# Kernel optimization log

Measured on AMD Instinct MI355X. Metric: run time of the kernel, lower is better.

The kernel has to match this reference:

```python
import jax, jax.numpy as jnp
import numpy as np
import math

K_HISTORY = 32  # sliding-window length over GRU hidden states


def rotate_half(x):
    half = x.shape[-1] // 2
    return jnp.concatenate([-x[..., half:], x[..., :half]], axis=-1)


def setup_inputs() -> dict:
    key = jax.random.key(0)
    ks = jax.random.split(key, 8)
    B, MB, IN = 8, 512, 1024          # batch, max_bin, input_size (gru_hidden_size)
    EMB, H, KVH, HD, BS = 1024, 16, 4, 64, 16  # embed_dim, heads, kv_heads, head_dim, bin_size
    h = jax.random.normal(ks[0], (B, MB, IN), jnp.float32)
    # RoPE tables: rotate-half layout, theta repeated over both halves
    pos = jnp.arange(MB, dtype=jnp.float32)
    inv_freq = 1.0 / (10000.0 ** (jnp.arange(0, HD, 2, dtype=jnp.float32) / HD))
    theta = pos[:, None] * inv_freq[None, :]            # (MB, HD/2)
    theta = jnp.concatenate([theta, theta], axis=-1)    # (MB, HD)
    freqs_cos = jnp.cos(theta)
    freqs_sin = jnp.sin(theta)
    s = 0.02
    Wq = jax.random.normal(ks[1], (EMB, H * HD), jnp.float32) * s
    Wk = jax.random.normal(ks[2], (IN, KVH * HD), jnp.float32) * s
    Wv = jax.random.normal(ks[3], (IN, KVH * HD), jnp.float32) * s
    Wo = jax.random.normal(ks[4], (H * HD, EMB), jnp.float32) * s
    output_queries = jax.random.normal(ks[5], (BS, EMB), jnp.float32)
    Wr = jax.random.normal(ks[6], (EMB, 2), jnp.float32) * s
    br = jnp.zeros((2,), jnp.float32)
    return {"h": h, "freqs_cos": freqs_cos, "freqs_sin": freqs_sin,
            "Wq": Wq, "Wk": Wk, "Wv": Wv, "Wo": Wo,
            "output_queries": output_queries, "Wr": Wr, "br": br}


def reference(h, freqs_cos, freqs_sin, Wq, Wk, Wv, Wo, output_queries, Wr, br):
    B, MB, IN = h.shape
    HD = freqs_cos.shape[1]
    H = Wq.shape[1] // HD
    KVH = Wk.shape[1] // HD
    n_rep = H // KVH
    BS = output_queries.shape[0]
    K = K_HISTORY

    # sliding windows over bins: window t covers h[t-K+1 : t+1] (zero left-pad)
    h_padded = jnp.concatenate([jnp.zeros((B, K - 1, IN), h.dtype), h], axis=1)
    idx = jnp.arange(MB)[:, None] + jnp.arange(K)[None, :]   # (MB, K)
    h_win = h_padded[:, idx, :]                              # (B, MB, K, IN)

    k = (h_win @ Wk).reshape(B, MB, K, KVH, HD)
    v = (h_win @ Wv).reshape(B, MB, K, KVH, HD)

    # queries: shared learned output queries, identical across batch & bins
    q = (output_queries @ Wq).reshape(BS, H, HD)             # (BS, H, HD)
    # RoPE on Q only (is_decoder=True) at within-bin offsets 0..BS-1
    offs = jnp.arange(BS)
    cos = freqs_cos[offs][:, None, :]                        # (BS, 1, HD)
    sin = freqs_sin[offs][:, None, :]
    q = q * cos + rotate_half(q) * sin                       # (BS, H, HD)

    # GQA: repeat_interleave KV heads to H heads
    k = jnp.repeat(k, n_rep, axis=3)                         # (B, MB, K, H, HD)
    v = jnp.repeat(v, n_rep, axis=3)

    scores = jnp.einsum("qhd,bmkhd->bmhqk", q, k) / math.sqrt(HD)
    attn = jax.nn.softmax(scores, axis=-1)                   # (B, MB, H, BS, K)
    attn_out = jnp.einsum("bmhqk,bmkhd->bmqhd", attn, v)
    attn_out = attn_out.reshape(B, MB, BS, H * HD)

    z = attn_out @ Wo                                        # (B, MB, BS, EMB)
    vel = z @ Wr + br                                        # (B, MB, BS, 2)
    return vel.reshape(B, MB * BS, 2)
```

## Files before the change

kernel.cpp:

```cpp
#include <hip/hip_runtime.h>


typedef __attribute__((ext_vector_type(8))) short v8s;
typedef __attribute__((ext_vector_type(4))) short v4sh;
typedef __attribute__((ext_vector_type(4))) float v4f;

#define OFF_WOR  0u
#define OFF_QR   2048u
#define OFF_WTH  18432u
#define OFF_WTL  182272u
#define OFF_S0   346112u
#define OFF_S1   1460224u
#define OFF_VW0  2574336u
#define OFF_VW1  2713600u
#define SROW 544

__device__ __forceinline__ void split_bf16(float a, unsigned short& h, unsigned short& l) {
    const unsigned u = __float_as_uint(a);
    h = (unsigned short)(u >> 16);
    const float r = a - __uint_as_float(u & 0xFFFF0000u);
    unsigned v = __float_as_uint(r);
    v += 0x7FFFu + ((v >> 16) & 1u);
    l = (unsigned short)(v >> 16);
}

__global__ __launch_bounds__(256) void kP(
    const float* __restrict__ oq, const float* __restrict__ Wq,
    const float* __restrict__ fc, const float* __restrict__ fs,
    const float* __restrict__ Wo, const float* __restrict__ Wr,
    float* __restrict__ qr, float* __restrict__ Wor,
    float* __restrict__ S0, float* __restrict__ S1,
    float* __restrict__ VW0, float* __restrict__ VW1,
    unsigned* __restrict__ wthu, unsigned* __restrict__ wtlu)
{
    __shared__ float sm[2048];
    const int b = blockIdx.x, t = threadIdx.x;
    if (b < 256) {
        const int q = b >> 4, h = b & 15;
        #pragma unroll
        for (int j = 0; j < 4; ++j) sm[t + 256 * j] = oq[q * 1024 + t + 256 * j];
        __syncthreads();
        const int w = t >> 6, lane = t & 63;
        const float* wq = Wq + (size_t)(w * 256) * 1024 + h * 64 + lane;
        const float* os = sm + w * 256;
        float acc = 0.f;
        #pragma unroll 16
        for (int e = 0; e < 256; ++e) acc = fmaf(os[e], wq[(size_t)e * 1024], acc);
        sm[1024 + w * 64 + lane] = acc;
        __syncthreads();
        if (t < 64) {
            const int d = t, p = d ^ 32;
            const float a1 = sm[1024 + d] + sm[1088 + d] + sm[1152 + d] + sm[1216 + d];
            const float a2 = sm[1024 + p] + sm[1088 + p] + sm[1152 + p] + sm[1216 + p];
            const float c = fc[q * 64 + d], s = fs[q * 64 + d];
            const float rh = (d < 32) ? -a2 : a2;
            qr[q * 1024 + h * 64 + d] = fmaf(a1, c, rh * s);
        }
    } else if (b < 512) {
        #pragma unroll
        for (int j = 0; j < 8; ++j) sm[t + 256 * j] = Wr[t + 256 * j];
        __syncthreads();
        const int i = (b - 256) * 4 + (t >> 6);
        const int lane = t & 63;
        float a0 = 0.f, a1 = 0.f;
        const float* wo = Wo + (size_t)i * 1024 + lane;
        #pragma unroll
        for (int j = 0; j < 16; ++j) {
            const float w = wo[j * 64];
            const int e = lane + j * 64;
            a0 = fmaf(w, sm[2 * e], a0);
            a1 = fmaf(w, sm[2 * e + 1], a1);
        }
        #pragma unroll
        for (int w = 1; w < 64; w <<= 1) {
            a0 += __shfl_xor(a0, w, 64);
            a1 += __shfl_xor(a1, w, 64);
        }
        if (lane == 0) { Wor[i * 2] = a0; Wor[i * 2 + 1] = a1; }
    } else if (b < 656) {
        const int idx = (b - 512) * 256 + t;
        const float4 z = make_float4(0.f, 0.f, 0.f, 0.f);
        if (idx < 16384)       *(float4*)(S0  + (size_t)(idx >> 3) * SROW + (idx & 7) * 4) = z;
        else if (idx < 32768)  *(float4*)(S1  + (size_t)((idx - 16384) >> 3) * SROW + (idx & 7) * 4) = z;
        else if (idx < 34816)  *(float4*)(VW0 + (size_t)((idx - 32768) >> 3) * SROW + (idx & 7) * 4) = z;
        else                   *(float4*)(VW1 + (size_t)((idx - 34816) >> 3) * SROW + (idx & 7) * 4) = z;
    } else {
        unsigned* dst = (b == 656) ? wthu : wtlu;
        #pragma unroll
        for (int j = 0; j < 64; ++j) dst[147456 + t + 256 * j] = 0u;
    }
}

__global__ __launch_bounds__(256) void kW(
    const float* __restrict__ Wk, const float* __restrict__ Wv,
    const float* __restrict__ qr, const float* __restrict__ Wor,
    unsigned short* __restrict__ Wth, unsigned short* __restrict__ Wtl)
{
    __shared__ float As[32 * 68];
    __shared__ float Bt[72 * 68];
    const int b = blockIdx.x, t = threadIdx.x;
    const int g = b >> 5, i0 = (b & 31) * 32;
    #pragma unroll
    for (int jj = 0; jj < 16; ++jj) {
        const int i2 = t + 256 * jj;
        const int d = i2 & 63, col = i2 >> 6;
        Bt[col * 68 + d] = qr[(col >> 2) * 1024 + (g * 4 + (col & 3)) * 64 + d];
    }
    #pragma unroll
    for (int jj = 0; jj < 2; ++jj) {
        const int i2 = t + 256 * jj;
        const int d = i2 & 63, vc = i2 >> 6;
        Bt[(64 + vc) * 68 + d] = Wor[((g * 4 + (vc >> 1)) * 64 + d) * 2 + (vc & 1)];
    }
    {
        const int i = t >> 3, dc = (t & 7) * 8;
        const float* src = Wk + (size_t)(i0 + i) * 256 + g * 64 + dc;
        *(float4*)&As[i * 68 + dc] = *(const float4*)src;
        *(float4*)&As[i * 68 + dc + 4] = *(const float4*)(src + 4);
    }
    __syncthreads();
    const int jc = t & 63, iq = t >> 6;
    {
        float out[8];
        #pragma unroll
        for (int r = 0; r < 8; ++r) out[r] = 0.f;
        #pragma unroll
        for (int dc = 0; dc < 16; ++dc) {
            const float4 bv = *(const float4*)&Bt[jc * 68 + dc * 4];
            #pragma unroll
            for (int r = 0; r < 8; ++r) {
                const float4 av = *(const float4*)&As[(iq * 8 + r) * 68 + dc * 4];
                out[r] = fmaf(av.x, bv.x, out[r]);
                out[r] = fmaf(av.y, bv.y, out[r]);
                out[r] = fmaf(av.z, bv.z, out[r]);
                out[r] = fmaf(av.w, bv.w, out[r]);
            }
        }
        const int j = (jc >> 2) * 16 + g * 4 + (jc & 3);
        v8s ph, pl;
        #pragma unroll
        for (int r = 0; r < 8; ++r) {
            unsigned short hh, ll;
            split_bf16(out[r] * 0.125f, hh, ll);
            ph[r] = (short)hh; pl[r] = (short)ll;
        }
        *(v8s*)&Wth[(size_t)j * 1024 + i0 + iq * 8] = ph;
        *(v8s*)&Wtl[(size_t)j * 1024 + i0 + iq * 8] = pl;
    }
    __syncthreads();
    {
        const int i = t >> 3, dc = (t & 7) * 8;
        const float* src = Wv + (size_t)(i0 + i) * 256 + g * 64 + dc;
        *(float4*)&As[i * 68 + dc] = *(const float4*)src;
        *(float4*)&As[i * 68 + dc + 4] = *(const float4*)(src + 4);
    }
    __syncthreads();
    {
        const int il = t >> 3, vc = t & 7;
        float acc = 0.f;
        #pragma unroll
        for (int dc = 0; dc < 16; ++dc) {
            const float4 av = *(const float4*)&As[il * 68 + dc * 4];
            const float4 bv = *(const float4*)&Bt[(64 + vc) * 68 + dc * 4];
            acc = fmaf(av.x, bv.x, acc);
            acc = fmaf(av.y, bv.y, acc);
            acc = fmaf(av.z, bv.z, acc);
            acc = fmaf(av.w, bv.w, acc);
        }
        const int j = 256 + (g * 4 + (vc >> 1)) * 2 + (vc & 1);
        unsigned short hh, ll;
        split_bf16(acc, hh, ll);
        Wth[(size_t)j * 1024 + i0 + il] = hh;
        Wtl[(size_t)j * 1024 + i0 + il] = ll;
    }
}

__global__ __launch_bounds__(256) void k2(
    const float* __restrict__ A,
    const unsigned short* __restrict__ Wth, const unsigned short* __restrict__ Wtl,
    float* __restrict__ S0, float* __restrict__ S1,
    float* __restrict__ VW0, float* __restrict__ VW1)
{
    __shared__ unsigned short Ah[64 * 72], Al[64 * 72];
    __shared__ unsigned short Bh[64 * 72], Bl[64 * 72];
    const int m0 = blockIdx.x * 64;
    const int n0 = blockIdx.y * 64;
    const int kh = blockIdx.z;
    const int t = threadIdx.x;
    const int lane = t & 63, wv = t >> 6;
    const int l16 = lane & 15, quad = lane >> 4;
    const int wm = wv >> 1, wn = wv & 1;
    const int sr = t >> 2, kc = (t & 3) * 8;
    v4f acc[2][2];
    #pragma unroll
    for (int i = 0; i < 2; ++i)
        #pragma unroll
        for (int j = 0; j < 2; ++j) acc[i][j] = (v4f)(0.f);
    const float* Ap = A + (size_t)(m0 + sr) * 1024 + kh * 512 + kc;
    const unsigned short* Bph = Wth + (size_t)(n0 + sr) * 1024 + kh * 512 + kc;
    const unsigned short* Bpl = Wtl + (size_t)(n0 + sr) * 1024 + kh * 512 + kc;
    for (int k0 = 0; k0 < 512; k0 += 64) {
        const float4 a00 = *(const float4*)(Ap + k0);
        const float4 a01 = *(const float4*)(Ap + k0 + 4);
        const float4 a10 = *(const float4*)(Ap + k0 + 32);
        const float4 a11 = *(const float4*)(Ap + k0 + 36);
        const v8s bh0 = *(const v8s*)(Bph + k0);
        const v8s bh1 = *(const v8s*)(Bph + k0 + 32);
        const v8s bl0 = *(const v8s*)(Bpl + k0);
        const v8s bl1 = *(const v8s*)(Bpl + k0 + 32);
        v8s ah0, al0, ah1, al1;
        {
            const float af0[8] = {a00.x, a00.y, a00.z, a00.w, a01.x, a01.y, a01.z, a01.w};
            const float af1[8] = {a10.x, a10.y, a10.z, a10.w, a11.x, a11.y, a11.z, a11.w};
            #pragma unroll
            for (int j = 0; j < 8; ++j) {
                unsigned short hh, ll;
                split_bf16(af0[j], hh, ll);
                ah0[j] = (short)hh; al0[j] = (short)ll;
                split_bf16(af1[j], hh, ll);
                ah1[j] = (short)hh; al1[j] = (short)ll;
            }
        }
        __syncthreads();
        *(v8s*)&Ah[sr * 72 + kc] = ah0;  *(v8s*)&Ah[sr * 72 + kc + 32] = ah1;
        *(v8s*)&Al[sr * 72 + kc] = al0;  *(v8s*)&Al[sr * 72 + kc + 32] = al1;
        *(v8s*)&Bh[sr * 72 + kc] = bh0;  *(v8s*)&Bh[sr * 72 + kc + 32] = bh1;
        *(v8s*)&Bl[sr * 72 + kc] = bl0;  *(v8s*)&Bl[sr * 72 + kc + 32] = bl1;
        __syncthreads();
        #pragma unroll
        for (int kk = 0; kk < 2; ++kk) {
            v8s fah[2], fal[2], fbh[2], fbl[2];
            #pragma unroll
            for (int s = 0; s < 2; ++s) {
                const int mr = wm * 32 + s * 16 + l16;
                fah[s] = *(const v8s*)&Ah[mr * 72 + kk * 32 + quad * 8];
                fal[s] = *(const v8s*)&Al[mr * 72 + kk * 32 + quad * 8];
                const int nr = wn * 32 + s * 16 + l16;
                fbh[s] = *(const v8s*)&Bh[nr * 72 + kk * 32 + quad * 8];
                fbl[s] = *(const v8s*)&Bl[nr * 72 + kk * 32 + quad * 8];
            }
            #pragma unroll
            for (int ms = 0; ms < 2; ++ms)
                #pragma unroll
                for (int ns = 0; ns < 2; ++ns) {
                    acc[ms][ns] = __builtin_amdgcn_mfma_f32_16x16x32_bf16(fal[ms], fbh[ns], acc[ms][ns], 0, 0, 0);
                    acc[ms][ns] = __builtin_amdgcn_mfma_f32_16x16x32_bf16(fah[ms], fbl[ns], acc[ms][ns], 0, 0, 0);
                    acc[ms][ns] = __builtin_amdgcn_mfma_f32_16x16x32_bf16(fah[ms], fbh[ns], acc[ms][ns], 0, 0, 0);
                }
        }
    }
    float* Sh  = kh ? S1 : S0;
    float* VWh = kh ? VW1 : VW0;
    #pragma unroll
    for (int ms = 0; ms < 2; ++ms)
        #pragma unroll
        for (int ns = 0; ns < 2; ++ns) {
            const int j = n0 + wn * 32 + ns * 16 + l16;
            if (j >= 288) continue;
            const int m = m0 + wm * 32 + ms * 16 + quad * 4;
            const int bb = m >> 9, tt = m & 511;
            const float4 v = make_float4(acc[ms][ns][0], acc[ms][ns][1], acc[ms][ns][2], acc[ms][ns][3]);
            float* dst;
            if (j < 256)
                dst = Sh + (size_t)((bb * 16 + (j >> 4)) * 16 + (j & 15)) * SROW + 32 + tt;
            else
                dst = VWh + (size_t)(bb * 32 + (j - 256)) * SROW + 32 + tt;
            *(float4*)dst = v;
        }
}

__global__ __launch_bounds__(256) void k3(
    const float* __restrict__ S0, const float* __restrict__ S1,
    const float* __restrict__ VW0, const float* __restrict__ VW1,
    const float* __restrict__ brp, float* __restrict__ out)
{
    __shared__ float Es[16 * 164];
    __shared__ float EVs[32 * 164];
    const int b = blockIdx.x, q = blockIdx.y, qt = blockIdx.z;
    const int tbase = qt * 128;
    const int t = threadIdx.x;
    for (int idx = t; idx < 640; idx += 256) {
        const int h = idx / 40, g = idx - h * 40;
        const size_t off = (size_t)((b * 16 + q) * 16 + h) * SROW + tbase + g * 4;
        const float4 a = *(const float4*)(S0 + off);
        const float4 c = *(const float4*)(S1 + off);
        float4 e;
        e.x = __expf(a.x + c.x); e.y = __expf(a.y + c.y);
        e.z = __expf(a.z + c.z); e.w = __expf(a.w + c.w);
        *(float4*)(Es + h * 164 + g * 4) = e;
    }
    __syncthreads();
    for (int idx = t; idx < 1280; idx += 256) {
        const int hc = idx / 40, g = idx - hc * 40;
        const size_t off = (size_t)(b * 32 + hc) * SROW + tbase + g * 4;
        const float4 v0 = *(const float4*)(VW0 + off);
        const float4 v1 = *(const float4*)(VW1 + off);
        const float4 e = *(const float4*)(Es + (hc >> 1) * 164 + g * 4);
        float4 rr;
        rr.x = e.x * (v0.x + v1.x); rr.y = e.y * (v0.y + v1.y);
        rr.z = e.z * (v0.z + v1.z); rr.w = e.w * (v0.w + v1.w);
        *(float4*)(EVs + hc * 164 + g * 4) = rr;
    }
    __syncthreads();
    const int h = t & 15, mg = t >> 4;
    const float* ep = Es + h * 164 + mg * 8;
    const float* e0 = EVs + (2 * h) * 164 + mg * 8;
    const float* e1 = EVs + (2 * h + 1) * 164 + mg * 8;
    float den = 0.f, n0s = 0.f, n1s = 0.f;
    #pragma unroll
    for (int s = 0; s < 32; ++s) {
        const int ss = 1 + ((s + 2 * h) & 31);
        den += ep[ss]; n0s += e0[ss]; n1s += e1[ss];
    }
    const float br0 = brp[0], br1 = brp[1];
    #pragma unroll
    for (int u = 0; u < 8; ++u) {
        const float inv = __builtin_amdgcn_rcpf(den);
        float c0 = n0s * inv, c1 = n1s * inv;
        #pragma unroll
        for (int w = 1; w < 16; w <<= 1) {
            c0 += __shfl_xor(c0, w, 64);
            c1 += __shfl_xor(c1, w, 64);
        }
        if (h == 0) {
            const int m = tbase + mg * 8 + u;
            float* o = out + (size_t)((b * 512 + m) * 16 + q) * 2;
            o[0] = c0 + br0;
            o[1] = c1 + br1;
        }
        if (u < 7) {
            den += ep[33 + u] - ep[1 + u];
            n0s += e0[33 + u] - e0[1 + u];
            n1s += e1[33 + u] - e1[1 + u];
        }
    }
}

extern "C" void kernel_launch(void* const* d_in, const int* in_sizes, int n_in,
                              void* d_out, int out_size, void* d_ws, size_t ws_size,
                              hipStream_t stream)
{
    (void)in_sizes; (void)n_in; (void)out_size; (void)ws_size;
    const float* h  = (const float*)d_in[0];
    const float* fc = (const float*)d_in[1];
    const float* fs = (const float*)d_in[2];
    const float* Wq = (const float*)d_in[3];
    const float* Wk = (const float*)d_in[4];
    const float* Wv = (const float*)d_in[5];
    const float* Wo = (const float*)d_in[6];
    const float* oq = (const float*)d_in[7];
    const float* Wr = (const float*)d_in[8];
    const float* br = (const float*)d_in[9];
    float* ws = (float*)d_ws;
    float* Wor  = ws + OFF_WOR;
    float* qr   = ws + OFF_QR;
    unsigned short* Wth = (unsigned short*)(ws + OFF_WTH);
    unsigned short* Wtl = (unsigned short*)(ws + OFF_WTL);
    float* S0   = ws + OFF_S0;
    float* S1   = ws + OFF_S1;
    float* VW0  = ws + OFF_VW0;
    float* VW1  = ws + OFF_VW1;
    float* out = (float*)d_out;

    hipLaunchKernelGGL(kP, dim3(658), dim3(256), 0, stream,
                       oq, Wq, fc, fs, Wo, Wr, qr, Wor, S0, S1, VW0, VW1,
                       (unsigned*)Wth, (unsigned*)Wtl);
    hipLaunchKernelGGL(kW, dim3(128), dim3(256), 0, stream, Wk, Wv, qr, Wor, Wth, Wtl);
    hipLaunchKernelGGL(k2, dim3(64, 5, 2), dim3(256), 0, stream, h, Wth, Wtl, S0, S1, VW0, VW1);
    hipLaunchKernelGGL(k3, dim3(8, 16, 4), dim3(256), 0, stream, S0, S1, VW0, VW1, br, out);
}
```

Before: 123.5 us.

## Pre-split h into bf16 hi/lo in prologue, prefetch k2 tiles, retile kW

Moves the fp32-to-bf16 hi/lo split of h out of the GEMM kernel k2 into extra blocks of the prologue kernel kP, which write two bf16 copies of h to workspace. k2 now loads pre-split bf16 tiles and software-prefetches the next K-slice into registers while the MFMA loop runs. kW is retiled to 16-row blocks with twice the grid so more blocks are in flight. The cost is an extra full pass over h (fp32 read plus two bf16 writes) and scalar stores in kW in exchange for a k2 inner loop with no conversion work and with overlapped loads.

```diff
diff --git a/kernel.cpp b/kernel.cpp
--- a/kernel.cpp
+++ b/kernel.cpp
@@ -2,7 +2,6 @@
 
 
 typedef __attribute__((ext_vector_type(8))) short v8s;
-typedef __attribute__((ext_vector_type(4))) short v4sh;
 typedef __attribute__((ext_vector_type(4))) float v4f;
 
 #define OFF_WOR  0u
@@ -13,6 +12,8 @@
 #define OFF_S1   1460224u
 #define OFF_VW0  2574336u
 #define OFF_VW1  2713600u
+#define OFF_AH   2852864u
+#define OFF_AL   4950016u
 #define SROW 544
 
 __device__ __forceinline__ void split_bf16(float a, unsigned short& h, unsigned short& l) {
@@ -28,13 +29,31 @@
     const float* __restrict__ oq, const float* __restrict__ Wq,
     const float* __restrict__ fc, const float* __restrict__ fs,
     const float* __restrict__ Wo, const float* __restrict__ Wr,
+    const float* __restrict__ hsrc,
     float* __restrict__ qr, float* __restrict__ Wor,
     float* __restrict__ S0, float* __restrict__ S1,
     float* __restrict__ VW0, float* __restrict__ VW1,
-    unsigned* __restrict__ wthu, unsigned* __restrict__ wtlu)
+    unsigned* __restrict__ wthu, unsigned* __restrict__ wtlu,
+    unsigned short* __restrict__ Ahg, unsigned short* __restrict__ Alg)
 {
     __shared__ float sm[2048];
     const int b = blockIdx.x, t = threadIdx.x;
+    if (b >= 658) {
+        const int base = (b - 658) * 2048 + t * 8;
+        const float4 x0 = *(const float4*)(hsrc + base);
+        const float4 x1 = *(const float4*)(hsrc + base + 4);
+        const float af[8] = {x0.x, x0.y, x0.z, x0.w, x1.x, x1.y, x1.z, x1.w};
+        v8s ah, al;
+        #pragma unroll
+        for (int j = 0; j < 8; ++j) {
+            unsigned short hh, ll;
+            split_bf16(af[j], hh, ll);
+            ah[j] = (short)hh; al[j] = (short)ll;
+        }
+        *(v8s*)(Ahg + base) = ah;
+        *(v8s*)(Alg + base) = al;
+        return;
+    }
     if (b < 256) {
         const int q = b >> 4, h = b & 15;
         #pragma unroll
@@ -96,10 +115,10 @@
     const float* __restrict__ qr, const float* __restrict__ Wor,
     unsigned short* __restrict__ Wth, unsigned short* __restrict__ Wtl)
 {
-    __shared__ float As[32 * 68];
+    __shared__ float As[16 * 68];
     __shared__ float Bt[72 * 68];
     const int b = blockIdx.x, t = threadIdx.x;
-    const int g = b >> 5, i0 = (b & 31) * 32;
+    const int g = b & 3, i0 = (b >> 2) * 16;
     #pragma unroll
     for (int jj = 0; jj < 16; ++jj) {
         const int i2 = t + 256 * jj;
@@ -113,49 +132,41 @@
         Bt[(64 + vc) * 68 + d] = Wor[((g * 4 + (vc >> 1)) * 64 + d) * 2 + (vc & 1)];
     }
     {
-        const int i = t >> 3, dc = (t & 7) * 8;
-        const float* src = Wk + (size_t)(i0 + i) * 256 + g * 64 + dc;
-        *(float4*)&As[i * 68 + dc] = *(const float4*)src;
-        *(float4*)&As[i * 68 + dc + 4] = *(const float4*)(src + 4);
+        const int i = t >> 4, dc = (t & 15) * 4;
+        *(float4*)&As[i * 68 + dc] = *(const float4*)(Wk + (size_t)(i0 + i) * 256 + g * 64 + dc);
     }
     __syncthreads();
     const int jc = t & 63, iq = t >> 6;
     {
-        float out[8];
-        #pragma unroll
-        for (int r = 0; r < 8; ++r) out[r] = 0.f;
+        float o4[4] = {0.f, 0.f, 0.f, 0.f};
         #pragma unroll
         for (int dc = 0; dc < 16; ++dc) {
             const float4 bv = *(const float4*)&Bt[jc * 68 + dc * 4];
             #pragma unroll
-            for (int r = 0; r < 8; ++r) {
-                const float4 av = *(const float4*)&As[(iq * 8 + r) * 68 + dc * 4];
-                out[r] = fmaf(av.x, bv.x, out[r]);
-                out[r] = fmaf(av.y, bv.y, out[r]);
-                out[r] = fmaf(av.z, bv.z, out[r]);
-                out[r] = fmaf(av.w, bv.w, out[r]);
+            for (int r = 0; r < 4; ++r) {
+                const float4 av = *(const float4*)&As[(iq * 4 + r) * 68 + dc * 4];
+                o4[r] = fmaf(av.x, bv.x, o4[r]);
+                o4[r] = fmaf(av.y, bv.y, o4[r]);
+                o4[r] = fmaf(av.z, bv.z, o4[r]);
+                o4[r] = fmaf(av.w, bv.w, o4[r]);
             }
         }
         const int j = (jc >> 2) * 16 + g * 4 + (jc & 3);
-        v8s ph, pl;
-        #pragma unroll
-        for (int r = 0; r < 8; ++r) {
+        #pragma unroll
+        for (int r = 0; r < 4; ++r) {
             unsigned short hh, ll;
-            split_bf16(out[r] * 0.125f, hh, ll);
-            ph[r] = (short)hh; pl[r] = (short)ll;
-        }
-        *(v8s*)&Wth[(size_t)j * 1024 + i0 + iq * 8] = ph;
-        *(v8s*)&Wtl[(size_t)j * 1024 + i0 + iq * 8] = pl;
+            split_bf16(o4[r] * 0.125f, hh, ll);
+            Wth[(size_t)j * 1024 + i0 + iq * 4 + r] = hh;
+            Wtl[(size_t)j * 1024 + i0 + iq * 4 + r] = ll;
+        }
     }
     __syncthreads();
     {
-        const int i = t >> 3, dc = (t & 7) * 8;
-        const float* src = Wv + (size_t)(i0 + i) * 256 + g * 64 + dc;
-        *(float4*)&As[i * 68 + dc] = *(const float4*)src;
-        *(float4*)&As[i * 68 + dc + 4] = *(const float4*)(src + 4);
-    }
-    __syncthreads();
-    {
+        const int i = t >> 4, dc = (t & 15) * 4;
+        *(float4*)&As[i * 68 + dc] = *(const float4*)(Wv + (size_t)(i0 + i) * 256 + g * 64 + dc);
+    }
+    __syncthreads();
+    if (t < 128) {
         const int il = t >> 3, vc = t & 7;
         float acc = 0.f;
         #pragma unroll
@@ -176,7 +187,7 @@
 }
 
 __global__ __launch_bounds__(256) void k2(
-    const float* __restrict__ A,
+    const unsigned short* __restrict__ Ahg, const unsigned short* __restrict__ Alg,
     const unsigned short* __restrict__ Wth, const unsigned short* __restrict__ Wtl,
     float* __restrict__ S0, float* __restrict__ S1,
     float* __restrict__ VW0, float* __restrict__ VW1)
@@ -196,37 +207,28 @@
     for (int i = 0; i < 2; ++i)
         #pragma unroll
         for (int j = 0; j < 2; ++j) acc[i][j] = (v4f)(0.f);
-    const float* Ap = A + (size_t)(m0 + sr) * 1024 + kh * 512 + kc;
+    const unsigned short* Aph = Ahg + (size_t)(m0 + sr) * 1024 + kh * 512 + kc;
+    const unsigned short* Apl = Alg + (size_t)(m0 + sr) * 1024 + kh * 512 + kc;
     const unsigned short* Bph = Wth + (size_t)(n0 + sr) * 1024 + kh * 512 + kc;
     const unsigned short* Bpl = Wtl + (size_t)(n0 + sr) * 1024 + kh * 512 + kc;
+    v8s rah0 = *(const v8s*)(Aph);      v8s rah1 = *(const v8s*)(Aph + 32);
+    v8s ral0 = *(const v8s*)(Apl);      v8s ral1 = *(const v8s*)(Apl + 32);
+    v8s rbh0 = *(const v8s*)(Bph);      v8s rbh1 = *(const v8s*)(Bph + 32);
+    v8s rbl0 = *(const v8s*)(Bpl);      v8s rbl1 = *(const v8s*)(Bpl + 32);
     for (int k0 = 0; k0 < 512; k0 += 64) {
-        const float4 a00 = *(const float4*)(Ap + k0);
-        const float4 a01 = *(const float4*)(Ap + k0 + 4);
-        const float4 a10 = *(const float4*)(Ap + k0 + 32);
-        const float4 a11 = *(const float4*)(Ap + k0 + 36);
-        const v8s bh0 = *(const v8s*)(Bph + k0);
-        const v8s bh1 = *(const v8s*)(Bph + k0 + 32);
-        const v8s bl0 = *(const v8s*)(Bpl + k0);
-        const v8s bl1 = *(const v8s*)(Bpl + k0 + 32);
-        v8s ah0, al0, ah1, al1;
-        {
-            const float af0[8] = {a00.x, a00.y, a00.z, a00.w, a01.x, a01.y, a01.z, a01.w};
-            const float af1[8] = {a10.x, a10.y, a10.z, a10.w, a11.x, a11.y, a11.z, a11.w};
-            #pragma unroll
-            for (int j = 0; j < 8; ++j) {
-                unsigned short hh, ll;
-                split_bf16(af0[j], hh, ll);
-                ah0[j] = (short)hh; al0[j] = (short)ll;
-                split_bf16(af1[j], hh, ll);
-                ah1[j] = (short)hh; al1[j] = (short)ll;
-            }
-        }
-        __syncthreads();
-        *(v8s*)&Ah[sr * 72 + kc] = ah0;  *(v8s*)&Ah[sr * 72 + kc + 32] = ah1;
-        *(v8s*)&Al[sr * 72 + kc] = al0;  *(v8s*)&Al[sr * 72 + kc + 32] = al1;
-        *(v8s*)&Bh[sr * 72 + kc] = bh0;  *(v8s*)&Bh[sr * 72 + kc + 32] = bh1;
-        *(v8s*)&Bl[sr * 72 + kc] = bl0;  *(v8s*)&Bl[sr * 72 + kc + 32] = bl1;
-        __syncthreads();
+        __syncthreads();
+        *(v8s*)&Ah[sr * 72 + kc] = rah0;  *(v8s*)&Ah[sr * 72 + kc + 32] = rah1;
+        *(v8s*)&Al[sr * 72 + kc] = ral0;  *(v8s*)&Al[sr * 72 + kc + 32] = ral1;
+        *(v8s*)&Bh[sr * 72 + kc] = rbh0;  *(v8s*)&Bh[sr * 72 + kc + 32] = rbh1;
+        *(v8s*)&Bl[sr * 72 + kc] = rbl0;  *(v8s*)&Bl[sr * 72 + kc + 32] = rbl1;
+        __syncthreads();
+        if (k0 + 64 < 512) {
+            const int kn = k0 + 64;
+            rah0 = *(const v8s*)(Aph + kn);  rah1 = *(const v8s*)(Aph + kn + 32);
+            ral0 = *(const v8s*)(Apl + kn);  ral1 = *(const v8s*)(Apl + kn + 32);
+            rbh0 = *(const v8s*)(Bph + kn);  rbh1 = *(const v8s*)(Bph + kn + 32);
+            rbl0 = *(const v8s*)(Bpl + kn);  rbl1 = *(const v8s*)(Bpl + kn + 32);
+        }
         #pragma unroll
         for (int kk = 0; kk < 2; ++kk) {
             v8s fah[2], fal[2], fbh[2], fbl[2];
@@ -360,12 +362,14 @@
     float* S1   = ws + OFF_S1;
     float* VW0  = ws + OFF_VW0;
     float* VW1  = ws + OFF_VW1;
+    unsigned short* Ahg = (unsigned short*)(ws + OFF_AH);
+    unsigned short* Alg = (unsigned short*)(ws + OFF_AL);
     float* out = (float*)d_out;
 
-    hipLaunchKernelGGL(kP, dim3(658), dim3(256), 0, stream,
-                       oq, Wq, fc, fs, Wo, Wr, qr, Wor, S0, S1, VW0, VW1,
-                       (unsigned*)Wth, (unsigned*)Wtl);
-    hipLaunchKernelGGL(kW, dim3(128), dim3(256), 0, stream, Wk, Wv, qr, Wor, Wth, Wtl);
-    hipLaunchKernelGGL(k2, dim3(64, 5, 2), dim3(256), 0, stream, h, Wth, Wtl, S0, S1, VW0, VW1);
+    hipLaunchKernelGGL(kP, dim3(2706), dim3(256), 0, stream,
+                       oq, Wq, fc, fs, Wo, Wr, h, qr, Wor, S0, S1, VW0, VW1,
+                       (unsigned*)Wth, (unsigned*)Wtl, Ahg, Alg);
+    hipLaunchKernelGGL(kW, dim3(256), dim3(256), 0, stream, Wk, Wv, qr, Wor, Wth, Wtl);
+    hipLaunchKernelGGL(k2, dim3(64, 5, 2), dim3(256), 0, stream, Ahg, Alg, Wth, Wtl, S0, S1, VW0, VW1);
     hipLaunchKernelGGL(k3, dim3(8, 16, 4), dim3(256), 0, stream, S0, S1, VW0, VW1, br, out);
 }
```

Result: no change. 122.3 us, median of 2 (-1.0%).
